# Performance work log

Measured on AMD Instinct MI355X. Metric: run time of the kernel, lower is better.

Reference implementation:

```python
import jax, jax.numpy as jnp
import numpy as np

B = 65536        # batch of class observations
NUM_CLASSES = 100
D = 128          # embedding_latent_dim / MLP width
H = 64           # rnn_hidden_dim == vq_embedding_dim (must match when use_vq)
K = 512          # vq_num_embeddings
S = 16           # num_splines
A = 6            # spline_action_dim
SQUISH = 0.2
BETA = 0.25      # vq commitment cost


def setup_inputs() -> dict:
    key = jax.random.key(0)
    ks = jax.random.split(key, 32)
    g = lambda i, shape, s=0.05: jax.random.normal(ks[i], shape, jnp.float32) * s
    return dict(
        obs=jax.random.randint(ks[0], (B,), 0, NUM_CLASSES, dtype=jnp.int32),
        embed=g(1, (NUM_CLASSES, D)),
        W1=g(2, (D, D)), b1=jnp.zeros((D,), jnp.float32),
        W2=g(3, (D, D)), b2=jnp.zeros((D,), jnp.float32),
        W3=g(4, (D, D)), b3=jnp.zeros((D,), jnp.float32),
        Wc=g(5, (D, H)), bc=jnp.zeros((H,), jnp.float32),      # carry_init
        Wi=g(6, (D, H)), bi=jnp.zeros((H,), jnp.float32),      # SimpleCell input dense
        Wh=g(7, (H, H)),                                       # SimpleCell recurrent (no bias)
        vq_emb=g(8, (K, H)),                                   # VQ codebook
        Wm=g(9, (H, A)), bm=jnp.zeros((A,), jnp.float32),      # actor mean head
        Ws=g(10, (H, A)), bs=jnp.zeros((A,), jnp.float32),     # actor scale head
        Vw1=g(11, (D, D)), vb1=jnp.zeros((D,), jnp.float32),
        Vw2=g(12, (D, D)), vb2=jnp.zeros((D,), jnp.float32),
        Vw3=g(13, (D, 32)), vb3=jnp.zeros((32,), jnp.float32),
        Vw4=g(14, (32, 1)), vb4=jnp.zeros((1,), jnp.float32),
    )


def reference(obs, embed, W1, b1, W2, b2, W3, b3, Wc, bc, Wi, bi, Wh, vq_emb,
              Wm, bm, Ws, bs, Vw1, vb1, Vw2, vb2, Vw3, vb3, Vw4, vb4):
    # class embedding + ReLU MLP trunk
    z = embed[obs]                                # (B, D)
    z = jax.nn.relu(z @ W1 + b1)
    z = jax.nn.relu(z @ W2 + b2)
    z = jax.nn.relu(z @ W3 + b3)

    carry0 = z @ Wc + bc                          # (B, H) initial RNN carry
    emb_sq = jnp.sum(vq_emb ** 2, axis=1)         # (K,) precomputed codebook norms

    def step(carry, _):
        # SimpleCell: h = tanh(Dense(inputs) + Dense_h(carry)); inputs = z each step
        h = jnp.tanh(z @ Wi + bi + carry @ Wh)    # (B, H)
        # VQ nearest-neighbor lookup
        d = jnp.sum(h ** 2, axis=1, keepdims=True) - 2.0 * (h @ vq_emb.T) + emb_sq  # (B, K)
        idx = jnp.argmin(d, axis=1)               # (B,)
        quant = jnp.take(vq_emb, idx, axis=0)     # (B, H) == one_hot(idx) @ vq_emb
        q = h + jax.lax.stop_gradient(quant - h)  # straight-through estimator
        e_loss = jnp.mean((jax.lax.stop_gradient(q) - h) ** 2)
        q_loss = jnp.mean((q - jax.lax.stop_gradient(h)) ** 2)
        vq_loss_i = q_loss + BETA * e_loss
        # spline heads (use_tanh_last=False -> sigmoid, temp=1)
        am = jax.nn.sigmoid(q @ Wm + bm)                    # (B, A)
        sd = jax.nn.sigmoid(q @ Ws + bs) * SQUISH + 1e-8    # (B, A)
        return q, (am, sd, vq_loss_i, idx)

    _, (ams, sds, losses, idxs) = jax.lax.scan(step, carry0, None, length=S)
    # (S, B, A) -> (B, S*A), matching concatenate along axis 1 in step order
    actor_mean = jnp.transpose(ams, (1, 0, 2)).reshape(B, S * A)
    actor_scale_diag = jnp.transpose(sds, (1, 0, 2)).reshape(B, S * A)

    # critic MLP (tanh activations)
    c = jnp.tanh(z @ Vw1 + vb1)
    c = jnp.tanh(c @ Vw2 + vb2)
    c = jnp.tanh(c @ Vw3 + vb3)
    critic = jnp.squeeze(c @ Vw4 + vb4, axis=-1)  # (B,)

    total_vq_loss = jnp.sum(losses)
    return actor_mean, actor_scale_diag, critic, total_vq_loss, idxs
```

## Files before the change

### kernel.cpp

```cpp
#include <hip/hip_runtime.h>
#include <cmath>


#define D_ 128
#define H_ 64
#define K_ 512
#define S_ 16
#define B_ 65536

#define OAM   ((size_t)0)
#define OSD   ((size_t)(B_ * 96))
#define OCRIT ((size_t)(2 * B_ * 96))
#define OLOSS ((size_t)(2 * B_ * 96 + B_))
#define OIDX  ((size_t)(2 * B_ * 96 + B_ + 1))

#define WS_VQWH   0
#define WS_AM8    (512 * 64)
#define WS_SD8    (WS_AM8 + 512 * 8)
#define WS_EMBSQ  (WS_SD8 + 512 * 8)
#define WS_CNT    (WS_EMBSQ + 512)
#define WS_CLIDX  (WS_CNT + 128)
#define WS_CLAM   (WS_CLIDX + 128 * 16)
#define WS_CLSD   (WS_CLAM + 128 * 96)
#define WS_CLCR   (WS_CLSD + 128 * 96)
#define WS_CLLOSS (WS_CLCR + 128)

typedef const __attribute__((address_space(1))) void GASV;
typedef __attribute__((address_space(3))) void LASV;
__device__ __forceinline__ void gll16(const void* g, void* l)
{
    __builtin_amdgcn_global_load_lds((GASV*)g, (LASV*)l, 16, 0, 0);
}

template <int N4>
__device__ __forceinline__ void dma_lin(float4* __restrict__ dst,
                                        const float4* __restrict__ src,
                                        int wid, int lane)
{
    constexpr int PER = N4 / 8;
#pragma unroll
    for (int j = 0; j < PER; j += 64) {
        const int f = wid * PER + j;
        gll16(src + f + lane, dst + f);
    }
}

__global__ __launch_bounds__(64) void table_kernel(
    const float* __restrict__ vq, const float* __restrict__ Wh,
    const float* __restrict__ Wm, const float* __restrict__ bm,
    const float* __restrict__ Ws, const float* __restrict__ bs,
    float* __restrict__ vqwh, float* __restrict__ am8,
    float* __restrict__ sd8, float* __restrict__ embsq,
    int* __restrict__ cnt)
{
    const int k = blockIdx.x;
    const int d = threadIdx.x;
    if (k < 2) cnt[k * 64 + d] = 0;

    __shared__ float er[64];
    er[d] = vq[k * 64 + d];
    __syncthreads();

    float acc = 0.f;
#pragma unroll 8
    for (int dd = 0; dd < 64; ++dd) acc = fmaf(er[dd], Wh[dd * 64 + d], acc);
    vqwh[k * 64 + d] = acc;

    float sq = er[d] * er[d];
#pragma unroll
    for (int m = 1; m < 64; m <<= 1) sq += __shfl_xor(sq, m);
    if (d == 0) embsq[k] = sq;

    if (d < 8) {
        float vm = 0.f, vs = 0.f;
        if (d < 6) {
            vm = bm[d];
            vs = bs[d];
            for (int dd = 0; dd < 64; ++dd) {
                vm = fmaf(er[dd], Wm[dd * 6 + d], vm);
                vs = fmaf(er[dd], Ws[dd * 6 + d], vs);
            }
            vm = 1.f / (1.f + expf(-vm));
            vs = 1.f / (1.f + expf(-vs)) * 0.2f + 1e-8f;
        }
        am8[k * 8 + d] = vm;
        sd8[k * 8 + d] = vs;
    }
}

__global__ __launch_bounds__(512)
__attribute__((amdgpu_waves_per_eu(2, 2)))
void class_kernel(
    const int* __restrict__ obs, int* __restrict__ cnt, int nclass,
    const float* __restrict__ embed,
    const float* __restrict__ W1, const float* __restrict__ b1,
    const float* __restrict__ W2, const float* __restrict__ b2,
    const float* __restrict__ W3, const float* __restrict__ b3,
    const float* __restrict__ Wc, const float* __restrict__ bc,
    const float* __restrict__ Wi, const float* __restrict__ bi,
    const float* __restrict__ Wh,
    const float* __restrict__ Vw1, const float* __restrict__ vb1,
    const float* __restrict__ Vw2, const float* __restrict__ vb2,
    const float* __restrict__ Vw3, const float* __restrict__ vb3,
    const float* __restrict__ Vw4, const float* __restrict__ vb4,
    const float* __restrict__ vqwh, const float* __restrict__ am8,
    const float* __restrict__ sd8, const float* __restrict__ embsq,
    const float* __restrict__ vq_emb,
    float* __restrict__ clam, float* __restrict__ clsd,
    float* __restrict__ clcr, float* __restrict__ clidx,
    float* __restrict__ clloss)
{
    extern __shared__ float4 dyn4[];
    float* __restrict__ Af    = reinterpret_cast<float*>(dyn4);
    float* __restrict__ Bf    = reinterpret_cast<float*>(dyn4 + 4096);
    float* __restrict__ vqwhL = reinterpret_cast<float*>(dyn4);
    __shared__ float zA[128], zB[128];
    __shared__ float psum[512];
    __shared__ float t1s[64], c0s[64], c3s[32];
    __shared__ float vw4s[32] __attribute__((aligned(16)));
    __shared__ float Wh_s[64 * 64] __attribute__((aligned(16)));
    __shared__ float hcand[2][4][64] __attribute__((aligned(16)));
    __shared__ float rD2[2][4];
    __shared__ int   rK2[2][4];
    __shared__ int   gk_s[16];
    __shared__ float gd_s[16];
    __shared__ float hh_s[16];

    const int c    = blockIdx.x;
    const int tid  = threadIdx.x;

    if (c >= nclass) {
        int* __restrict__ hsh = reinterpret_cast<int*>(psum);
        if (tid < 128) hsh[tid] = 0;
        __syncthreads();
        const int hb = c - nclass;
        for (int i = hb * 512 + tid; i < B_; i += 16 * 512)
            atomicAdd(&hsh[obs[i]], 1);
        __syncthreads();
        if (tid < 128) {
            const int v = hsh[tid];
            if (v) atomicAdd(&cnt[tid], v);
        }
        return;
    }

    const int lane = tid & 63;
    const int wid  = tid >> 6;
    const float4* __restrict__ vq4   = reinterpret_cast<const float4*>(vq_emb);
    const float4* __restrict__ vqwh4 = reinterpret_cast<const float4*>(vqwh);

    const int j128 = tid & 127;
    const int q4   = tid >> 7;

    dma_lin<4096>(dyn4, reinterpret_cast<const float4*>(W1), wid, lane);
    if (tid < 128) zA[tid] = embed[c * 128 + tid];
    __syncthreads();

#define DENSE128(SRCW, ZSRC, ZDST, BIAS, ACT)                                  \
    {                                                                          \
        float a0 = 0.f, a1 = 0.f, a2 = 0.f, a3 = 0.f;                          \
        const int i0 = q4 * 32;                                                \
        _Pragma("unroll 8")                                                    \
        for (int ii = 0; ii < 32; ii += 4) {                                   \
            a0 = fmaf(ZSRC[i0 + ii + 0], SRCW[(i0 + ii + 0) * 128 + j128], a0);\
            a1 = fmaf(ZSRC[i0 + ii + 1], SRCW[(i0 + ii + 1) * 128 + j128], a1);\
            a2 = fmaf(ZSRC[i0 + ii + 2], SRCW[(i0 + ii + 2) * 128 + j128], a2);\
            a3 = fmaf(ZSRC[i0 + ii + 3], SRCW[(i0 + ii + 3) * 128 + j128], a3);\
        }                                                                      \
        psum[q4 * 128 + j128] = (a0 + a1) + (a2 + a3);                         \
    }                                                                          \
    __syncthreads();                                                           \
    if (tid < 128) {                                                           \
        float v = BIAS[tid] + ((psum[tid] + psum[128 + tid]) +                 \
                               (psum[256 + tid] + psum[384 + tid]));           \
        ZDST[tid] = ACT;                                                       \
    }                                                                          \
    __syncthreads();

    dma_lin<4096>(dyn4 + 4096, reinterpret_cast<const float4*>(W2), wid, lane);
    DENSE128(Af, zA, zB, b1, fmaxf(v, 0.f))

    dma_lin<4096>(dyn4, reinterpret_cast<const float4*>(W3), wid, lane);
    DENSE128(Bf, zB, zA, b2, fmaxf(v, 0.f))

    dma_lin<2048>(dyn4 + 4096, reinterpret_cast<const float4*>(Wi), wid, lane);
    dma_lin<2048>(dyn4 + 6144, reinterpret_cast<const float4*>(Wc), wid, lane);
    DENSE128(Af, zA, zB, b3, fmaxf(v, 0.f))

    dma_lin<4096>(dyn4, vqwh4, wid, lane);
    dma_lin<1024>(reinterpret_cast<float4*>(Wh_s),
                  reinterpret_cast<const float4*>(Wh), wid, lane);
    {
        const int jj = tid & 63;
        const int qq = (tid >> 6) & 3;
        const bool isC = tid >= 256;
        const float* __restrict__ Wsrc = isC ? (Bf + 8192) : Bf;
        float a0 = 0.f, a1 = 0.f, a2 = 0.f, a3 = 0.f;
        const int i0 = qq * 32;
#pragma unroll 8
        for (int ii = 0; ii < 32; ii += 4) {
            a0 = fmaf(zB[i0 + ii + 0], Wsrc[(i0 + ii + 0) * 64 + jj], a0);
            a1 = fmaf(zB[i0 + ii + 1], Wsrc[(i0 + ii + 1) * 64 + jj], a1);
            a2 = fmaf(zB[i0 + ii + 2], Wsrc[(i0 + ii + 2) * 64 + jj], a2);
            a3 = fmaf(zB[i0 + ii + 3], Wsrc[(i0 + ii + 3) * 64 + jj], a3);
        }
        psum[(isC ? 256 : 0) + qq * 64 + jj] = (a0 + a1) + (a2 + a3);
    }
    __syncthreads();

    dma_lin<4096>(dyn4 + 4096, vqwh4 + 4096, wid, lane);
    if (tid < 64) {
        t1s[tid] = bi[tid] + ((psum[tid] + psum[64 + tid]) +
                              (psum[128 + tid] + psum[192 + tid]));
    } else if (tid < 128) {
        const int j = tid - 64;
        c0s[j] = bc[j] + ((psum[256 + j] + psum[320 + j]) +
                          (psum[384 + j] + psum[448 + j]));
    } else if (tid < 160) {
        vw4s[tid - 128] = Vw4[tid - 128];
    }
    __syncthreads();

    {
        const int j = lane;
        const int q = wid;
        float a0 = 0.f, a1 = 0.f;
        const int i0 = q * 8;
#pragma unroll
        for (int ii = 0; ii < 8; ii += 2) {
            a0 = fmaf(c0s[i0 + ii + 0], Wh_s[(i0 + ii + 0) * 64 + j], a0);
            a1 = fmaf(c0s[i0 + ii + 1], Wh_s[(i0 + ii + 1) * 64 + j], a1);
        }
        psum[q * 64 + j] = a0 + a1;
    }
    float4 cb[16], cb2[16];
    float esq = 0.f, esq2 = 0.f;
    if (wid < 4) {
        const float4* __restrict__ r1 = vq4 + (size_t)tid * 16;
        const float4* __restrict__ r2 = vq4 + (size_t)(tid + 256) * 16;
#pragma unroll
        for (int d4 = 0; d4 < 16; ++d4) { cb[d4] = r1[d4]; cb2[d4] = r2[d4]; }
#pragma unroll
        for (int d4 = 0; d4 < 16; ++d4) {
            asm volatile("" : "+v"(cb[d4].x), "+v"(cb[d4].y),
                              "+v"(cb[d4].z), "+v"(cb[d4].w));
            asm volatile("" : "+v"(cb2[d4].x), "+v"(cb2[d4].y),
                              "+v"(cb2[d4].z), "+v"(cb2[d4].w));
        }
        esq  = embsq[tid];
        esq2 = embsq[tid + 256];
    }
    __syncthreads();

    if (tid < 64) {
        float a = 0.f;
#pragma unroll
        for (int q = 0; q < 8; ++q) a += psum[q * 64 + tid];
        hcand[0][0][tid] = tanhf(a + t1s[tid]);
    }
    const float t1r = t1s[lane];
    __syncthreads();

    if (wid == 0) {
        const float h0v = hcand[0][0][lane];
        float hh = h0v * h0v;
#pragma unroll
        for (int m = 1; m < 64; m <<= 1) hh += __shfl_xor(hh, m);
        if (lane == 0) hh_s[0] = hh;
    }

    int prevw = 0;
    float ca0 = 0.f, ca1 = 0.f, ca2 = 0.f, ca3 = 0.f;
#pragma unroll 1
    for (int t = 0; t < S_; ++t) {
        const int buf = t & 1;
        if (wid < 4) {
            const float* __restrict__ cur = hcand[buf][prevw];
            float a0 = 0.f, a1 = 0.f, a2 = 0.f, a3 = 0.f;
            float b0 = 0.f, b1_ = 0.f, b2_ = 0.f, b3_ = 0.f;
#pragma unroll
            for (int d4 = 0; d4 < 16; d4 += 4) {
                const float4 h0v = *reinterpret_cast<const float4*>(cur + 4 * d4);
                a0 = fmaf(h0v.x, cb[d4].x, a0); a0 = fmaf(h0v.y, cb[d4].y, a0);
                a0 = fmaf(h0v.z, cb[d4].z, a0); a0 = fmaf(h0v.w, cb[d4].w, a0);
                b0 = fmaf(h0v.x, cb2[d4].x, b0); b0 = fmaf(h0v.y, cb2[d4].y, b0);
                b0 = fmaf(h0v.z, cb2[d4].z, b0); b0 = fmaf(h0v.w, cb2[d4].w, b0);
                const float4 h1v = *reinterpret_cast<const float4*>(cur + 4 * d4 + 4);
                a1 = fmaf(h1v.x, cb[d4 + 1].x, a1); a1 = fmaf(h1v.y, cb[d4 + 1].y, a1);
                a1 = fmaf(h1v.z, cb[d4 + 1].z, a1); a1 = fmaf(h1v.w, cb[d4 + 1].w, a1);
                b1_ = fmaf(h1v.x, cb2[d4 + 1].x, b1_); b1_ = fmaf(h1v.y, cb2[d4 + 1].y, b1_);
                b1_ = fmaf(h1v.z, cb2[d4 + 1].z, b1_); b1_ = fmaf(h1v.w, cb2[d4 + 1].w, b1_);
                const float4 h2v = *reinterpret_cast<const float4*>(cur + 4 * d4 + 8);
                a2 = fmaf(h2v.x, cb[d4 + 2].x, a2); a2 = fmaf(h2v.y, cb[d4 + 2].y, a2);
                a2 = fmaf(h2v.z, cb[d4 + 2].z, a2); a2 = fmaf(h2v.w, cb[d4 + 2].w, a2);
                b2_ = fmaf(h2v.x, cb2[d4 + 2].x, b2_); b2_ = fmaf(h2v.y, cb2[d4 + 2].y, b2_);
                b2_ = fmaf(h2v.z, cb2[d4 + 2].z, b2_); b2_ = fmaf(h2v.w, cb2[d4 + 2].w, b2_);
                const float4 h3v = *reinterpret_cast<const float4*>(cur + 4 * d4 + 12);
                a3 = fmaf(h3v.x, cb[d4 + 3].x, a3); a3 = fmaf(h3v.y, cb[d4 + 3].y, a3);
                a3 = fmaf(h3v.z, cb[d4 + 3].z, a3); a3 = fmaf(h3v.w, cb[d4 + 3].w, a3);
                b3_ = fmaf(h3v.x, cb2[d4 + 3].x, b3_); b3_ = fmaf(h3v.y, cb2[d4 + 3].y, b3_);
                b3_ = fmaf(h3v.z, cb2[d4 + 3].z, b3_); b3_ = fmaf(h3v.w, cb2[d4 + 3].w, b3_);
            }
            const float d1 = fmaf(-2.f, (a0 + a1) + (a2 + a3), esq);
            const float d2 = fmaf(-2.f, (b0 + b1_) + (b2_ + b3_), esq2);
            float bD = d1;
            int   bK = tid;
            if (d2 < bD) { bD = d2; bK = tid + 256; }
#pragma unroll
            for (int m = 1; m < 64; m <<= 1) {
                const float od = __shfl_xor(bD, m);
                const int   ok = __shfl_xor(bK, m);
                if (od < bD || (od == bD && ok < bK)) { bD = od; bK = ok; }
            }
            const float vw = vqwhL[(bK << 6) + lane];
            hcand[buf ^ 1][wid][lane] = tanhf(t1r + vw);
            if (lane == 0) { rD2[buf][wid] = bD; rK2[buf][wid] = bK; }
        } else {
            const int u = tid - 256;
            const int j = u & 127;
            const int hf = u >> 7;
            if (t == 0 || t == 1 || t == 3 || t == 4) {
                const float* __restrict__ W = (t <= 1) ? Vw1 : Vw2;
                const float* __restrict__ zsrc = (t <= 1) ? zB : zA;
                const int i0 = 64 * hf + ((t == 1 || t == 4) ? 32 : 0);
                if (t == 0 || t == 3) { ca0 = ca1 = ca2 = ca3 = 0.f; }
#pragma unroll 8
                for (int ii = 0; ii < 32; ii += 4) {
                    ca0 = fmaf(zsrc[i0 + ii + 0], W[(i0 + ii + 0) * 128 + j], ca0);
                    ca1 = fmaf(zsrc[i0 + ii + 1], W[(i0 + ii + 1) * 128 + j], ca1);
                    ca2 = fmaf(zsrc[i0 + ii + 2], W[(i0 + ii + 2) * 128 + j], ca2);
                    ca3 = fmaf(zsrc[i0 + ii + 3], W[(i0 + ii + 3) * 128 + j], ca3);
                }
                if (t == 1 || t == 4) psum[u] = (ca0 + ca1) + (ca2 + ca3);
            } else if (t == 2) {
                if (u < 128) zA[u] = tanhf(vb1[u] + psum[u] + psum[128 + u]);
            } else if (t == 5) {
                if (u < 128) zA[u] = tanhf(vb2[u] + psum[u] + psum[128 + u]);
            } else if (t == 6) {
                const int j2 = u & 31;
                const int o  = u >> 5;
                float x0 = 0.f, x1 = 0.f;
                const int i0 = 16 * o;
#pragma unroll
                for (int ii = 0; ii < 16; ii += 2) {
                    x0 = fmaf(zA[i0 + ii + 0], Vw3[(i0 + ii + 0) * 32 + j2], x0);
                    x1 = fmaf(zA[i0 + ii + 1], Vw3[(i0 + ii + 1) * 32 + j2], x1);
                }
                psum[u] = x0 + x1;
            } else if (t == 7) {
                if (u < 32) {
                    float v = vb3[u];
#pragma unroll
                    for (int o = 0; o < 8; ++o) v += psum[o * 32 + u];
                    c3s[u] = tanhf(v);
                }
            } else if (t == 8) {
                if (u == 0) {
                    float sm = vb4[0];
#pragma unroll
                    for (int i = 0; i < 32; ++i) sm = fmaf(c3s[i], vw4s[i], sm);
                    clcr[c] = sm;
                }
            }
        }
        __syncthreads();

        float gD = rD2[buf][0];
        int   gK = rK2[buf][0], winw = 0;
#pragma unroll
        for (int w = 1; w < 4; ++w)
            if (rD2[buf][w] < gD || (rD2[buf][w] == gD && rK2[buf][w] < gK)) {
                gD = rD2[buf][w]; gK = rK2[buf][w]; winw = w;
            }
        if (tid == 0) { gk_s[t] = gK; gd_s[t] = gD; }
        prevw = winw;
    }
    __syncthreads();

    for (int tt = wid + 1; tt < S_; tt += 8) {
        const int g = gk_s[tt - 1];
        const float hv = tanhf(t1r + vqwhL[(g << 6) + lane]);
        float hh = hv * hv;
#pragma unroll
        for (int m = 1; m < 64; m <<= 1) hh += __shfl_xor(hh, m);
        if (lane == 0) hh_s[tt] = hh;
    }
    __syncthreads();
    if (tid == 0) {
        float s = 0.f;
#pragma unroll
        for (int t = 0; t < S_; ++t) s += gd_s[t] + hh_s[t];
        clloss[c] = s;
    }

    if (tid < 96) {
        const int t = tid / 6;
        const int j = tid - t * 6;
        const int gk = gk_s[t];
        clam[c * 96 + tid] = am8[gk * 8 + j];
        clsd[c * 96 + tid] = sd8[gk * 8 + j];
    } else if (tid >= 96 && tid < 112) {
        const int t = tid - 96;
        clidx[c * 16 + t] = (float)gk_s[t];
    }
}

__global__ __launch_bounds__(256) void scatter_kernel(
    const int* __restrict__ obs, const float* __restrict__ clam,
    const float* __restrict__ clsd, const float* __restrict__ clcr,
    const float* __restrict__ clidx, const int* __restrict__ cnt,
    const float* __restrict__ clloss, int nclass, float* __restrict__ out)
{
    if (blockIdx.x == 0 && threadIdx.x == 0) {
        float s = 0.f;
        for (int c = 0; c < nclass; ++c) s += (float)cnt[c] * clloss[c];
        out[OLOSS] = s * 1.25f / (65536.f * 64.f);
    }

    const int n_am4 = B_ * 24;
    const int n_cr4 = B_ / 4;
    const int n_idx = B_ * 16;
    const int tot   = 2 * n_am4 + n_cr4 + n_idx;
    float4* __restrict__ out4 = reinterpret_cast<float4*>(out);

    for (int i = blockIdx.x * 256 + threadIdx.x; i < tot; i += gridDim.x * 256) {
        if (i < 2 * n_am4) {
            const bool in_am = (i < n_am4);
            const int  i4    = in_am ? i : i - n_am4;
            const uint32_t row =
                (uint32_t)(((uint64_t)(i4 >> 3) * 0xAAAAAAABull) >> 33);
            const int col4 = i4 - (int)row * 24;
            const int cc   = obs[row];
            const float* __restrict__ tab = in_am ? clam : clsd;
            out4[i] = *reinterpret_cast<const float4*>(tab + cc * 96 + col4 * 4);
        } else if (i < 2 * n_am4 + n_cr4) {
            const int j = i - 2 * n_am4;
            const int r = 4 * j;
            float4 v;
            v.x = clcr[obs[r + 0]];
            v.y = clcr[obs[r + 1]];
            v.z = clcr[obs[r + 2]];
            v.w = clcr[obs[r + 3]];
            out4[i] = v;
        } else {
            const int j = i - (2 * n_am4 + n_cr4);
            const int t = j >> 16;
            const int r = j & (B_ - 1);
            out[OIDX + (size_t)j] = clidx[obs[r] * 16 + t];
        }
    }
}

extern "C" void kernel_launch(void* const* d_in, const int* in_sizes, int n_in,
                              void* d_out, int out_size, void* d_ws, size_t ws_size,
                              hipStream_t stream)
{
    const int*   obs   = (const int*)  d_in[0];
    const float* embed = (const float*)d_in[1];
    const float* W1    = (const float*)d_in[2];
    const float* b1    = (const float*)d_in[3];
    const float* W2    = (const float*)d_in[4];
    const float* b2    = (const float*)d_in[5];
    const float* W3    = (const float*)d_in[6];
    const float* b3    = (const float*)d_in[7];
    const float* Wc    = (const float*)d_in[8];
    const float* bc    = (const float*)d_in[9];
    const float* Wi    = (const float*)d_in[10];
    const float* bi    = (const float*)d_in[11];
    const float* Wh    = (const float*)d_in[12];
    const float* vq    = (const float*)d_in[13];
    const float* Wm    = (const float*)d_in[14];
    const float* bm    = (const float*)d_in[15];
    const float* Ws    = (const float*)d_in[16];
    const float* bs    = (const float*)d_in[17];
    const float* Vw1   = (const float*)d_in[18];
    const float* vb1   = (const float*)d_in[19];
    const float* Vw2   = (const float*)d_in[20];
    const float* vb2   = (const float*)d_in[21];
    const float* Vw3   = (const float*)d_in[22];
    const float* vb3   = (const float*)d_in[23];
    const float* Vw4   = (const float*)d_in[24];
    const float* vb4   = (const float*)d_in[25];

    const int nclass = in_sizes[1] / D_;

    float* ws_f   = (float*)d_ws;
    float* vqwh   = ws_f + WS_VQWH;
    float* am8    = ws_f + WS_AM8;
    float* sd8    = ws_f + WS_SD8;
    float* embsq  = ws_f + WS_EMBSQ;
    int*   cnt    = (int*)(ws_f + WS_CNT);
    float* clidx  = ws_f + WS_CLIDX;
    float* clam   = ws_f + WS_CLAM;
    float* clsd   = ws_f + WS_CLSD;
    float* clcr   = ws_f + WS_CLCR;
    float* clloss = ws_f + WS_CLLOSS;

    float* out = (float*)d_out;

    table_kernel<<<512, 64, 0, stream>>>(vq, Wh, Wm, bm, Ws, bs,
                                         vqwh, am8, sd8, embsq, cnt);
    class_kernel<<<nclass + 16, 512, 131072, stream>>>(
        obs, cnt, nclass,
        embed, W1, b1, W2, b2, W3, b3, Wc, bc, Wi, bi, Wh,
        Vw1, vb1, Vw2, vb2, Vw3, vb3, Vw4, vb4,
        vqwh, am8, sd8, embsq, vq,
        clam, clsd, clcr, clidx, clloss);
    scatter_kernel<<<2048, 256, 0, stream>>>(obs, clam, clsd, clcr, clidx,
                                             cnt, clloss, nclass, out);
}
```

Before: 59.58 us.

## Fuse codebook table build into class kernel with flag-based intra-grid sync

Removes the separate table_kernel launch by computing the VQ codebook tables (vq@Wh, norms, spline head sigmoids) in 64 extra blocks of the class kernel. Class blocks run their MLP trunk first and spin on a global counter before loading the tables, so table building overlaps the trunk. The histogram blocks now write per-block partial counts instead of using global atomics, which removes the need to zero the counts beforehand; the scatter kernel sums the partials and resets the flag. This relies on all table blocks being co-resident or scheduled ahead of the spinning blocks, which holds since they have lower block indices and the grid is small.

```diff
diff --git a/kernel.cpp b/kernel.cpp
--- a/kernel.cpp
+++ b/kernel.cpp
@@ -7,6 +7,8 @@
 #define K_ 512
 #define S_ 16
 #define B_ 65536
+#define NTBL_ 64
+#define NH_ 16
 
 #define OAM   ((size_t)0)
 #define OSD   ((size_t)(B_ * 96))
@@ -18,12 +20,14 @@
 #define WS_AM8    (512 * 64)
 #define WS_SD8    (WS_AM8 + 512 * 8)
 #define WS_EMBSQ  (WS_SD8 + 512 * 8)
-#define WS_CNT    (WS_EMBSQ + 512)
-#define WS_CLIDX  (WS_CNT + 128)
+#define WS_CNTP   (WS_EMBSQ + 512)
+#define WS_CLIDX  (WS_CNTP + 2048)
 #define WS_CLAM   (WS_CLIDX + 128 * 16)
 #define WS_CLSD   (WS_CLAM + 128 * 96)
 #define WS_CLCR   (WS_CLSD + 128 * 96)
 #define WS_CLLOSS (WS_CLCR + 128)
+
+__device__ int g_tflag = 0;
 
 typedef const __attribute__((address_space(1))) void GASV;
 typedef __attribute__((address_space(3))) void LASV;
@@ -45,53 +49,10 @@
     }
 }
 
-__global__ __launch_bounds__(64) void table_kernel(
-    const float* __restrict__ vq, const float* __restrict__ Wh,
-    const float* __restrict__ Wm, const float* __restrict__ bm,
-    const float* __restrict__ Ws, const float* __restrict__ bs,
-    float* __restrict__ vqwh, float* __restrict__ am8,
-    float* __restrict__ sd8, float* __restrict__ embsq,
-    int* __restrict__ cnt)
-{
-    const int k = blockIdx.x;
-    const int d = threadIdx.x;
-    if (k < 2) cnt[k * 64 + d] = 0;
-
-    __shared__ float er[64];
-    er[d] = vq[k * 64 + d];
-    __syncthreads();
-
-    float acc = 0.f;
-#pragma unroll 8
-    for (int dd = 0; dd < 64; ++dd) acc = fmaf(er[dd], Wh[dd * 64 + d], acc);
-    vqwh[k * 64 + d] = acc;
-
-    float sq = er[d] * er[d];
-#pragma unroll
-    for (int m = 1; m < 64; m <<= 1) sq += __shfl_xor(sq, m);
-    if (d == 0) embsq[k] = sq;
-
-    if (d < 8) {
-        float vm = 0.f, vs = 0.f;
-        if (d < 6) {
-            vm = bm[d];
-            vs = bs[d];
-            for (int dd = 0; dd < 64; ++dd) {
-                vm = fmaf(er[dd], Wm[dd * 6 + d], vm);
-                vs = fmaf(er[dd], Ws[dd * 6 + d], vs);
-            }
-            vm = 1.f / (1.f + expf(-vm));
-            vs = 1.f / (1.f + expf(-vs)) * 0.2f + 1e-8f;
-        }
-        am8[k * 8 + d] = vm;
-        sd8[k * 8 + d] = vs;
-    }
-}
-
 __global__ __launch_bounds__(512)
 __attribute__((amdgpu_waves_per_eu(2, 2)))
 void class_kernel(
-    const int* __restrict__ obs, int* __restrict__ cnt, int nclass,
+    const int* __restrict__ obs, int* __restrict__ cnt_part, int nclass,
     const float* __restrict__ embed,
     const float* __restrict__ W1, const float* __restrict__ b1,
     const float* __restrict__ W2, const float* __restrict__ b2,
@@ -99,12 +60,14 @@
     const float* __restrict__ Wc, const float* __restrict__ bc,
     const float* __restrict__ Wi, const float* __restrict__ bi,
     const float* __restrict__ Wh,
+    const float* __restrict__ Wm, const float* __restrict__ bm,
+    const float* __restrict__ Wsw, const float* __restrict__ bs,
     const float* __restrict__ Vw1, const float* __restrict__ vb1,
     const float* __restrict__ Vw2, const float* __restrict__ vb2,
     const float* __restrict__ Vw3, const float* __restrict__ vb3,
     const float* __restrict__ Vw4, const float* __restrict__ vb4,
-    const float* __restrict__ vqwh, const float* __restrict__ am8,
-    const float* __restrict__ sd8, const float* __restrict__ embsq,
+    float* __restrict__ vqwh, float* __restrict__ am8,
+    float* __restrict__ sd8, float* __restrict__ embsq,
     const float* __restrict__ vq_emb,
     float* __restrict__ clam, float* __restrict__ clsd,
     float* __restrict__ clcr, float* __restrict__ clidx,
@@ -126,26 +89,65 @@
     __shared__ float gd_s[16];
     __shared__ float hh_s[16];
 
-    const int c    = blockIdx.x;
+    const int bx   = blockIdx.x;
     const int tid  = threadIdx.x;
-
-    if (c >= nclass) {
+    const int lane = tid & 63;
+    const int wid  = tid >> 6;
+
+    if (bx < NTBL_) {
+        float* __restrict__ er = reinterpret_cast<float*>(dyn4) + wid * 64;
+        const int k = bx * 8 + wid;
+        er[lane] = vq_emb[k * 64 + lane];
+        __syncthreads();
+
+        float acc = 0.f;
+#pragma unroll 8
+        for (int dd = 0; dd < 64; ++dd)
+            acc = fmaf(er[dd], Wh[dd * 64 + lane], acc);
+        vqwh[k * 64 + lane] = acc;
+
+        float sq = er[lane] * er[lane];
+#pragma unroll
+        for (int m = 1; m < 64; m <<= 1) sq += __shfl_xor(sq, m);
+        if (lane == 0) embsq[k] = sq;
+
+        if (lane < 8) {
+            float vm = 0.f, vs = 0.f;
+            if (lane < 6) {
+                vm = bm[lane];
+                vs = bs[lane];
+                for (int dd = 0; dd < 64; ++dd) {
+                    vm = fmaf(er[dd], Wm[dd * 6 + lane], vm);
+                    vs = fmaf(er[dd], Wsw[dd * 6 + lane], vs);
+                }
+                vm = 1.f / (1.f + expf(-vm));
+                vs = 1.f / (1.f + expf(-vs)) * 0.2f + 1e-8f;
+            }
+            am8[k * 8 + lane] = vm;
+            sd8[k * 8 + lane] = vs;
+        }
+        __syncthreads();
+        if (tid == 0) {
+            __threadfence();
+            __hip_atomic_fetch_add(&g_tflag, 1, __ATOMIC_RELEASE,
+                                   __HIP_MEMORY_SCOPE_AGENT);
+        }
+        return;
+    }
+
+    if (bx < NTBL_ + NH_) {
         int* __restrict__ hsh = reinterpret_cast<int*>(psum);
         if (tid < 128) hsh[tid] = 0;
         __syncthreads();
-        const int hb = c - nclass;
-        for (int i = hb * 512 + tid; i < B_; i += 16 * 512)
+        const int hb = bx - NTBL_;
+        for (int i = hb * 512 + tid; i < B_; i += NH_ * 512)
             atomicAdd(&hsh[obs[i]], 1);
         __syncthreads();
-        if (tid < 128) {
-            const int v = hsh[tid];
-            if (v) atomicAdd(&cnt[tid], v);
-        }
+        if (tid < 128) cnt_part[hb * 128 + tid] = hsh[tid];
         return;
     }
 
-    const int lane = tid & 63;
-    const int wid  = tid >> 6;
+    const int c = bx - NTBL_ - NH_;
     const float4* __restrict__ vq4   = reinterpret_cast<const float4*>(vq_emb);
     const float4* __restrict__ vqwh4 = reinterpret_cast<const float4*>(vqwh);
 
@@ -186,6 +188,14 @@
     dma_lin<2048>(dyn4 + 4096, reinterpret_cast<const float4*>(Wi), wid, lane);
     dma_lin<2048>(dyn4 + 6144, reinterpret_cast<const float4*>(Wc), wid, lane);
     DENSE128(Af, zA, zB, b3, fmaxf(v, 0.f))
+
+    if (tid == 0) {
+        while (__hip_atomic_load(&g_tflag, __ATOMIC_RELAXED,
+                                 __HIP_MEMORY_SCOPE_AGENT) < NTBL_)
+            __builtin_amdgcn_s_sleep(2);
+        __builtin_amdgcn_fence(__ATOMIC_ACQUIRE, "agent");
+    }
+    __syncthreads();
 
     dma_lin<4096>(dyn4, vqwh4, wid, lane);
     dma_lin<1024>(reinterpret_cast<float4*>(Wh_s),
@@ -408,13 +418,28 @@
 __global__ __launch_bounds__(256) void scatter_kernel(
     const int* __restrict__ obs, const float* __restrict__ clam,
     const float* __restrict__ clsd, const float* __restrict__ clcr,
-    const float* __restrict__ clidx, const int* __restrict__ cnt,
+    const float* __restrict__ clidx, const int* __restrict__ cnt_part,
     const float* __restrict__ clloss, int nclass, float* __restrict__ out)
 {
-    if (blockIdx.x == 0 && threadIdx.x == 0) {
-        float s = 0.f;
-        for (int c = 0; c < nclass; ++c) s += (float)cnt[c] * clloss[c];
-        out[OLOSS] = s * 1.25f / (65536.f * 64.f);
+    __shared__ int icc_s[128];
+    if (blockIdx.x == 0) {
+        if (threadIdx.x == 0)
+            __hip_atomic_store(&g_tflag, 0, __ATOMIC_RELAXED,
+                               __HIP_MEMORY_SCOPE_AGENT);
+        if (threadIdx.x < 128) {
+            int cc = 0;
+#pragma unroll
+            for (int p = 0; p < NH_; ++p)
+                cc += cnt_part[p * 128 + threadIdx.x];
+            icc_s[threadIdx.x] = cc;
+        }
+        __syncthreads();
+        if (threadIdx.x == 0) {
+            float s = 0.f;
+            for (int c = 0; c < nclass; ++c)
+                s += (float)icc_s[c] * clloss[c];
+            out[OLOSS] = s * 1.25f / (65536.f * 64.f);
+        }
     }
 
     const int n_am4 = B_ * 24;
@@ -484,28 +509,27 @@
 
     const int nclass = in_sizes[1] / D_;
 
-    float* ws_f   = (float*)d_ws;
-    float* vqwh   = ws_f + WS_VQWH;
-    float* am8    = ws_f + WS_AM8;
-    float* sd8    = ws_f + WS_SD8;
-    float* embsq  = ws_f + WS_EMBSQ;
-    int*   cnt    = (int*)(ws_f + WS_CNT);
-    float* clidx  = ws_f + WS_CLIDX;
-    float* clam   = ws_f + WS_CLAM;
-    float* clsd   = ws_f + WS_CLSD;
-    float* clcr   = ws_f + WS_CLCR;
-    float* clloss = ws_f + WS_CLLOSS;
+    float* ws_f     = (float*)d_ws;
+    float* vqwh     = ws_f + WS_VQWH;
+    float* am8      = ws_f + WS_AM8;
+    float* sd8      = ws_f + WS_SD8;
+    float* embsq    = ws_f + WS_EMBSQ;
+    int*   cnt_part = (int*)(ws_f + WS_CNTP);
+    float* clidx    = ws_f + WS_CLIDX;
+    float* clam     = ws_f + WS_CLAM;
+    float* clsd     = ws_f + WS_CLSD;
+    float* clcr     = ws_f + WS_CLCR;
+    float* clloss   = ws_f + WS_CLLOSS;
 
     float* out = (float*)d_out;
 
-    table_kernel<<<512, 64, 0, stream>>>(vq, Wh, Wm, bm, Ws, bs,
-                                         vqwh, am8, sd8, embsq, cnt);
-    class_kernel<<<nclass + 16, 512, 131072, stream>>>(
-        obs, cnt, nclass,
+    class_kernel<<<NTBL_ + NH_ + nclass, 512, 131072, stream>>>(
+        obs, cnt_part, nclass,
         embed, W1, b1, W2, b2, W3, b3, Wc, bc, Wi, bi, Wh,
+        Wm, bm, Ws, bs,
         Vw1, vb1, Vw2, vb2, Vw3, vb3, Vw4, vb4,
         vqwh, am8, sd8, embsq, vq,
         clam, clsd, clcr, clidx, clloss);
     scatter_kernel<<<2048, 256, 0, stream>>>(obs, clam, clsd, clcr, clidx,
-                                             cnt, clloss, nclass, out);
+                                             cnt_part, clloss, nclass, out);
 }
```

After: 59.34 us. About the same (-0.4%).
